# Kernel tuning notes

Measured on AMD Instinct MI355X. Metric: run time of the kernel, lower is better.

The kernel has to match this reference:

```python
import jax, jax.numpy as jnp
import numpy as np

B, V, E, H, L = 1024, 50257, 512, 512, 2


def setup_inputs() -> dict:
    key = jax.random.key(0)
    ks = jax.random.split(key, 12)
    s = 1.0 / np.sqrt(H)
    inp = {
        "x": jax.random.randint(ks[0], (B,), 0, V),
        "hidden": jnp.zeros((2 * L, B, H), jnp.float32),
        "embed": jax.random.normal(ks[1], (V, E), jnp.float32) * 0.02,
        # layer 0: input size E; layer 1: input size 2H (bidirectional concat)
        "Wih0": jax.random.uniform(ks[2], (2, 3 * H, E), jnp.float32, -s, s),
        "Whh0": jax.random.uniform(ks[3], (2, 3 * H, H), jnp.float32, -s, s),
        "bih0": jax.random.uniform(ks[4], (2, 3 * H), jnp.float32, -s, s),
        "bhh0": jax.random.uniform(ks[5], (2, 3 * H), jnp.float32, -s, s),
        "Wih1": jax.random.uniform(ks[6], (2, 3 * H, 2 * H), jnp.float32, -s, s),
        "Whh1": jax.random.uniform(ks[7], (2, 3 * H, H), jnp.float32, -s, s),
        "bih1": jax.random.uniform(ks[8], (2, 3 * H), jnp.float32, -s, s),
        "bhh1": jax.random.uniform(ks[9], (2, 3 * H), jnp.float32, -s, s),
        "Wproj": jax.random.uniform(ks[10], (V, E), jnp.float32, -1.0 / np.sqrt(E), 1.0 / np.sqrt(E)),
        "bproj": jax.random.uniform(ks[11], (V,), jnp.float32, -1.0 / np.sqrt(E), 1.0 / np.sqrt(E)),
    }
    return inp


def _gru_cell(x, h, Wih, Whh, bih, bhh):
    # PyTorch GRU cell: gates ordered (r, z, n)
    gi = x @ Wih.T + bih            # [B, 3H]
    gh = h @ Whh.T + bhh            # [B, 3H]
    ir, iz, inn = jnp.split(gi, 3, axis=-1)
    hr, hz, hn = jnp.split(gh, 3, axis=-1)
    r = jax.nn.sigmoid(ir + hr)
    z = jax.nn.sigmoid(iz + hz)
    n = jnp.tanh(inn + r * hn)
    return (1.0 - z) * n + z * h


def reference(x, hidden, embed, Wih0, Whh0, bih0, bhh0, Wih1, Whh1, bih1, bhh1, Wproj, bproj):
    inp = embed[x]                  # [B, E] embedding lookup; seq_len == 1
    layer_params = [(Wih0, Whh0, bih0, bhh0), (Wih1, Whh1, bih1, bhh1)]
    new_h = []
    for l, (Wih, Whh, bih, bhh) in enumerate(layer_params):
        # single timestep: fwd and bwd directions each do one cell step on the same input
        hf = _gru_cell(inp, hidden[2 * l],     Wih[0], Whh[0], bih[0], bhh[0])
        hb = _gru_cell(inp, hidden[2 * l + 1], Wih[1], Whh[1], bih[1], bhh[1])
        new_h += [hf, hb]
        inp = jnp.concatenate([hf, hb], axis=-1)   # [B, 2H]
    # x[:, :, hidden_dim:] -> backward-direction output of top layer, then transpose(0,1)
    out = hb[:, None, :]                            # [B, 1, H]
    logits = out @ Wproj.T + bproj                  # [B, 1, V]
    probs = jax.nn.softmax(logits, axis=-1)
    return probs, jnp.stack(new_h, axis=0)          # ([B,1,V], [2L, B, H])
```

## Files before the change

### kernel.cpp

```cpp
#include <hip/hip_runtime.h>


#define Bsz 1024
#define Hs  512
#define Vv  50257
#define VP  50304
#define NG  1536
#define NPB 393

typedef __bf16 bf16x8 __attribute__((ext_vector_type(8)));
typedef float  floatx4 __attribute__((ext_vector_type(4)));

__device__ __forceinline__ unsigned short f2bf(float f) {
  unsigned int u = __builtin_bit_cast(unsigned int, f);
  u += 0x7fffu + ((u >> 16) & 1u);
  return (unsigned short)(u >> 16);
}

__device__ __forceinline__ float bf2f(unsigned short u) {
  unsigned int x = (unsigned int)u << 16;
  return __builtin_bit_cast(float, x);
}

__device__ __forceinline__ void cvt4(const float* src, unsigned short* dst) {
  float4 f = *(const float4*)src;
  unsigned int lo = (unsigned int)f2bf(f.x) | ((unsigned int)f2bf(f.y) << 16);
  unsigned int hi = (unsigned int)f2bf(f.z) | ((unsigned int)f2bf(f.w) << 16);
  *(uint2*)dst = make_uint2(lo, hi);
}

__device__ __forceinline__ void g2lds16(const void* g, void* l) {
  unsigned long long gv = (unsigned long long)g;
  unsigned int lv = (unsigned int)(unsigned long long)l;
  __builtin_amdgcn_global_load_lds(
      (const __attribute__((address_space(1))) unsigned int*)gv,
      (__attribute__((address_space(3))) unsigned int*)lv,
      16, 0, 0);
}

__device__ __forceinline__ void gemm_core8(const unsigned short* A, const unsigned short* Bw, int K,
                                           int mt, int nt,
                                           unsigned short* Alds, unsigned short* Blds,
                                           floatx4 (&acc)[4][4]) {
  const int tid = threadIdx.x;
  const int w = tid >> 6, l = tid & 63;
  const int wr = w >> 1, wc = w & 1;
  const int g = l >> 4, r16 = l & 15;
  floatx4 zero = {0.f, 0.f, 0.f, 0.f};
#pragma unroll
  for (int i = 0; i < 4; ++i)
#pragma unroll
    for (int j = 0; j < 4; ++j) acc[i][j] = zero;

  const int nsteps = K >> 6;
  for (int kt = 0; kt < nsteps; ++kt) {
    __syncthreads();
#pragma unroll
    for (int i = 0; i < 4; ++i) {
      int chunk = w * 4 + i;
      int t16 = chunk * 64 + l;
      int row = t16 >> 3, c = t16 & 7;
      int sc = c ^ (row & 7);
      g2lds16(A + (size_t)(mt * 256 + row) * K + kt * 64 + sc * 8, (char*)Alds + chunk * 1024);
    }
#pragma unroll
    for (int i = 0; i < 2; ++i) {
      int chunk = w * 2 + i;
      int t16 = chunk * 64 + l;
      int row = t16 >> 3, c = t16 & 7;
      int sc = c ^ (row & 7);
      g2lds16(Bw + (size_t)(nt * 128 + row) * K + kt * 64 + sc * 8, (char*)Blds + chunk * 1024);
    }
    __syncthreads();
#pragma unroll
    for (int ks = 0; ks < 2; ++ks) {
      bf16x8 a[4], b[4];
#pragma unroll
      for (int i = 0; i < 4; ++i) {
        int rowA = wr * 64 + i * 16 + r16;
        int ca = (ks * 4 + g) ^ (rowA & 7);
        a[i] = *(const bf16x8*)((const char*)Alds + rowA * 128 + ca * 16);
        int rowB = wc * 64 + i * 16 + r16;
        int cb = (ks * 4 + g) ^ (rowB & 7);
        b[i] = *(const bf16x8*)((const char*)Blds + rowB * 128 + cb * 16);
      }
#pragma unroll
      for (int i = 0; i < 4; ++i)
#pragma unroll
        for (int j = 0; j < 4; ++j)
          acc[i][j] = __builtin_amdgcn_mfma_f32_16x16x32_bf16(a[i], b[j], acc[i][j], 0, 0, 0);
    }
  }
}

struct GemmDesc {
  const unsigned short* A[4];
  const unsigned short* Bw[4];
  const float* bias[4];
  float* C[4];
  int K[4];
};

__global__ __launch_bounds__(512, 4) void gemm_gru_batch(GemmDesc d) {
  __shared__ alignas(16) unsigned short Alds[256 * 64];
  __shared__ alignas(16) unsigned short Blds[128 * 64];
  const int z = blockIdx.z;
  floatx4 acc[4][4];
  gemm_core8(d.A[z], d.Bw[z], d.K[z], blockIdx.y, blockIdx.x, Alds, Blds, acc);
  const float* bias = d.bias[z];
  float* C = d.C[z];
  const int tid = threadIdx.x, w = tid >> 6, l = tid & 63;
  const int wr = w >> 1, wc = w & 1, g = l >> 4, r16 = l & 15;
#pragma unroll
  for (int i = 0; i < 4; ++i)
#pragma unroll
    for (int j = 0; j < 4; ++j) {
      int col = blockIdx.x * 128 + wc * 64 + j * 16 + r16;
      float bc = bias[col];
#pragma unroll
      for (int q = 0; q < 4; ++q) {
        int row = blockIdx.y * 256 + wr * 64 + i * 16 + g * 4 + q;
        C[(size_t)row * NG + col] = acc[i][j][q] + bc;
      }
    }
}

template <int MODE>
__global__ __launch_bounds__(512, 4) void gemm_proj(const unsigned short* A, const unsigned short* Bw,
                                                    const float* biasp, unsigned short* stash,
                                                    float* probs, float* partial, const float* inv) {
  __shared__ alignas(16) unsigned short Alds[256 * 64];
  __shared__ alignas(16) unsigned short Blds[128 * 64];
  __shared__ float rowpart[256];
  const int tid = threadIdx.x;
  if (MODE != 2 && tid < 256) rowpart[tid] = 0.f;
  int orig = blockIdx.x;
  int xcd = orig & 7, slot = orig >> 3;
  int wgid = (xcd < 4 ? xcd * 197 : 788 + (xcd - 4) * 196) + slot;
  int mt = wgid & 3, nt = wgid >> 2;
  floatx4 acc[4][4];
  gemm_core8(A, Bw, 512, mt, nt, Alds, Blds, acc);
  const int w = tid >> 6, l = tid & 63;
  const int wr = w >> 1, wc = w & 1, g = l >> 4, r16 = l & 15;
  float bcol[4];
#pragma unroll
  for (int j = 0; j < 4; ++j) bcol[j] = biasp[nt * 128 + wc * 64 + j * 16 + r16];
#pragma unroll
  for (int i = 0; i < 4; ++i)
#pragma unroll
    for (int q = 0; q < 4; ++q) {
      int rowl = wr * 64 + i * 16 + g * 4 + q;
      int grow = mt * 256 + rowl;
      float rinv = (MODE == 2) ? inv[grow] : 0.f;
      float s = 0.f;
#pragma unroll
      for (int j = 0; j < 4; ++j) {
        int col = nt * 128 + wc * 64 + j * 16 + r16;
        float v = __expf(acc[i][j][q] + bcol[j]);
        if (MODE == 0) stash[(size_t)grow * VP + col] = f2bf(v);
        if (MODE == 2) { if (col < Vv) probs[(size_t)grow * Vv + col] = v * rinv; }
        s += v;
      }
      if (MODE != 2) {
        s += __shfl_xor(s, 1); s += __shfl_xor(s, 2);
        s += __shfl_xor(s, 4); s += __shfl_xor(s, 8);
        if (r16 == 0) atomicAdd(&rowpart[rowl], s);
      }
    }
  if (MODE != 2) {
    __syncthreads();
    if (tid < 256) partial[(size_t)(mt * 256 + tid) * NPB + nt] = rowpart[tid];
  }
}

__global__ __launch_bounds__(256) void gru_gates(const float* Cbuf, const float* hidden,
                                                 float* out_newh, unsigned short* bf_out, int layer) {
  int idx = blockIdx.x * 256 + threadIdx.x;
  int j = idx & 511;
  int b = (idx >> 9) & 1023;
  int d = idx >> 19;
  const float* GI = Cbuf + (size_t)d * Bsz * NG;
  const float* GH = Cbuf + (size_t)(2 + d) * Bsz * NG;
  size_t base = (size_t)b * NG + j;
  float ir = GI[base], iz = GI[base + 512], inn = GI[base + 1024];
  float hr = GH[base], hz = GH[base + 512], hn = GH[base + 1024];
  float r = 1.f / (1.f + __expf(-(ir + hr)));
  float z = 1.f / (1.f + __expf(-(iz + hz)));
  float n = tanhf(inn + r * hn);
  size_t hoff = (size_t)(2 * layer + d) * (Bsz * Hs) + (size_t)b * Hs + j;
  float hprev = hidden[hoff];
  float h = (1.f - z) * n + z * hprev;
  out_newh[hoff] = h;
  if (layer == 0) {
    bf_out[(size_t)b * 1024 + d * 512 + j] = f2bf(h);
  } else if (d == 1) {
    bf_out[(size_t)b * 512 + j] = f2bf(h);
  }
}

__global__ void convert_all(const float* Wih0, const float* Whh0, const float* Wih1, const float* Whh1,
                            const float* hidden, const float* Wproj, const float* bproj,
                            unsigned short* wih0b, unsigned short* whh0b, unsigned short* wih1b,
                            unsigned short* whh1b, unsigned short* hbf, unsigned short* wprojb,
                            float* bprojp) {
  long long idx = ((long long)blockIdx.x * 256 + threadIdx.x) * 4;
  if (idx < 1572864) { cvt4(Wih0 + idx, wih0b + idx); return; }
  idx -= 1572864;
  if (idx < 1572864) { cvt4(Whh0 + idx, whh0b + idx); return; }
  idx -= 1572864;
  if (idx < 3145728) { cvt4(Wih1 + idx, wih1b + idx); return; }
  idx -= 3145728;
  if (idx < 1572864) { cvt4(Whh1 + idx, whh1b + idx); return; }
  idx -= 1572864;
  if (idx < 2097152) { cvt4(hidden + idx, hbf + idx); return; }
  idx -= 2097152;
  if (idx < 25755648) {
    long long row = idx >> 9, col = idx & 511;
    if (row < Vv) cvt4(Wproj + row * 512 + col, wprojb + idx);
    else *(uint2*)(wprojb + idx) = make_uint2(0u, 0u);
    return;
  }
  idx -= 25755648;
  if (idx < VP) {
    float4 v;
    v.x = (idx + 0 < Vv) ? bproj[idx + 0] : -1e30f;
    v.y = (idx + 1 < Vv) ? bproj[idx + 1] : -1e30f;
    v.z = (idx + 2 < Vv) ? bproj[idx + 2] : -1e30f;
    v.w = (idx + 3 < Vv) ? bproj[idx + 3] : -1e30f;
    *(float4*)(bprojp + idx) = v;
  }
}

__global__ void gather_embed(const int* x, const float* embed, unsigned short* xe) {
  int b = blockIdx.x, t = threadIdx.x;
  int tok = x[b];
  float2 v = *(const float2*)(embed + (size_t)tok * 512 + t * 2);
  unsigned int o = ((unsigned int)f2bf(v.y) << 16) | f2bf(v.x);
  *(unsigned int*)((unsigned short*)xe + (size_t)b * 512 + t * 2) = o;
}

__global__ void rowsum_inv(const float* partial, float* inv) {
  int row = blockIdx.x, tid = threadIdx.x;
  float s = 0.f;
  for (int c = tid; c < NPB; c += 128) s += partial[(size_t)row * NPB + c];
  __shared__ float tmp[128];
  tmp[tid] = s;
  __syncthreads();
  for (int off = 64; off > 0; off >>= 1) {
    if (tid < off) tmp[tid] += tmp[tid + off];
    __syncthreads();
  }
  if (tid == 0) inv[row] = 1.0f / tmp[0];
}

__global__ __launch_bounds__(256) void scale_expand(const unsigned short* stash, const float* inv,
                                                    float* probs) {
  const unsigned int nquad = 12865792u;
  const unsigned int step = gridDim.x * 256u;
  for (unsigned int f = blockIdx.x * 256u + threadIdx.x; f < nquad; f += step) {
    unsigned int e0 = f * 4u;
    unsigned int row = e0 / (unsigned int)Vv;
    int col = (int)(e0 - row * (unsigned int)Vv);
    float4 o;
    if (col + 4 <= Vv) {
      float s = inv[row];
      const unsigned short* sp = stash + (size_t)row * VP + col;
      if ((col & 1) == 0) {
        unsigned int u0 = *(const unsigned int*)sp;
        unsigned int u1 = *(const unsigned int*)(sp + 2);
        o.x = bf2f((unsigned short)u0) * s;
        o.y = bf2f((unsigned short)(u0 >> 16)) * s;
        o.z = bf2f((unsigned short)u1) * s;
        o.w = bf2f((unsigned short)(u1 >> 16)) * s;
      } else {
        o.x = bf2f(sp[0]) * s; o.y = bf2f(sp[1]) * s;
        o.z = bf2f(sp[2]) * s; o.w = bf2f(sp[3]) * s;
      }
    } else {
      float vals[4];
#pragma unroll
      for (int k = 0; k < 4; ++k) {
        unsigned int e = e0 + k;
        unsigned int rk = e / (unsigned int)Vv;
        int ck = (int)(e - rk * (unsigned int)Vv);
        vals[k] = bf2f(stash[(size_t)rk * VP + ck]) * inv[rk];
      }
      o.x = vals[0]; o.y = vals[1]; o.z = vals[2]; o.w = vals[3];
    }
    *(float4*)(probs + e0) = o;
  }
}

extern "C" void kernel_launch(void* const* d_in, const int* in_sizes, int n_in,
                              void* d_out, int out_size, void* d_ws, size_t ws_size,
                              hipStream_t stream) {
  const int*   x      = (const int*)d_in[0];
  const float* hidden = (const float*)d_in[1];
  const float* embed  = (const float*)d_in[2];
  const float* Wih0   = (const float*)d_in[3];
  const float* Whh0   = (const float*)d_in[4];
  const float* bih0   = (const float*)d_in[5];
  const float* bhh0   = (const float*)d_in[6];
  const float* Wih1   = (const float*)d_in[7];
  const float* Whh1   = (const float*)d_in[8];
  const float* bih1   = (const float*)d_in[9];
  const float* bhh1   = (const float*)d_in[10];
  const float* Wproj  = (const float*)d_in[11];
  const float* bproj  = (const float*)d_in[12];
  float* out = (float*)d_out;

  char* ws = (char*)d_ws;
  unsigned short* wih0b  = (unsigned short*)(ws);
  unsigned short* whh0b  = (unsigned short*)(ws + 3145728);
  unsigned short* wih1b  = (unsigned short*)(ws + 6291456);
  unsigned short* whh1b  = (unsigned short*)(ws + 12582912);
  unsigned short* hbf    = (unsigned short*)(ws + 15728640);
  unsigned short* wprojb = (unsigned short*)(ws + 19922944);
  float*          bprojp = (float*)(ws + 71434240);
  unsigned short* xe     = (unsigned short*)(ws + 71635456);
  unsigned short* inp1   = (unsigned short*)(ws + 72684032);
  unsigned short* hb1    = (unsigned short*)(ws + 74781184);
  float*          Cbuf   = (float*)(ws + 75829760);
  float*          partial= (float*)(ws + 100995584);
  float*          inv    = (float*)(ws + 102605312);
  unsigned short* stash  = (unsigned short*)(ws + 102609408);
  const size_t NEED_STASH = 102609408ull + (size_t)Bsz * VP * 2ull;

  float* out_newh = out + 51463168ll;

  convert_all<<<34930, 256, 0, stream>>>(Wih0, Whh0, Wih1, Whh1, hidden, Wproj, bproj,
                                         wih0b, whh0b, wih1b, whh1b, hbf, wprojb, bprojp);
  gather_embed<<<1024, 256, 0, stream>>>(x, embed, xe);

  GemmDesc d0;
  d0.A[0] = xe;  d0.A[1] = xe;
  d0.A[2] = hbf; d0.A[3] = hbf + 524288;
  d0.Bw[0] = wih0b; d0.Bw[1] = wih0b + 786432;
  d0.Bw[2] = whh0b; d0.Bw[3] = whh0b + 786432;
  d0.bias[0] = bih0; d0.bias[1] = bih0 + 1536;
  d0.bias[2] = bhh0; d0.bias[3] = bhh0 + 1536;
  d0.C[0] = Cbuf;             d0.C[1] = Cbuf + 1572864;
  d0.C[2] = Cbuf + 2*1572864; d0.C[3] = Cbuf + 3*1572864;
  d0.K[0] = d0.K[1] = d0.K[2] = d0.K[3] = 512;
  gemm_gru_batch<<<dim3(12, 4, 4), 512, 0, stream>>>(d0);
  gru_gates<<<4096, 256, 0, stream>>>(Cbuf, hidden, out_newh, inp1, 0);

  GemmDesc d1;
  d1.A[0] = inp1; d1.A[1] = inp1;
  d1.A[2] = hbf + 2*524288; d1.A[3] = hbf + 3*524288;
  d1.Bw[0] = wih1b; d1.Bw[1] = wih1b + 1572864;
  d1.Bw[2] = whh1b; d1.Bw[3] = whh1b + 786432;
  d1.bias[0] = bih1; d1.bias[1] = bih1 + 1536;
  d1.bias[2] = bhh1; d1.bias[3] = bhh1 + 1536;
  d1.C[0] = Cbuf;             d1.C[1] = Cbuf + 1572864;
  d1.C[2] = Cbuf + 2*1572864; d1.C[3] = Cbuf + 3*1572864;
  d1.K[0] = d1.K[1] = 1024; d1.K[2] = d1.K[3] = 512;
  gemm_gru_batch<<<dim3(12, 4, 4), 512, 0, stream>>>(d1);
  gru_gates<<<4096, 256, 0, stream>>>(Cbuf, hidden, out_newh, hb1, 1);

  if (ws_size >= NEED_STASH) {
    gemm_proj<0><<<1572, 512, 0, stream>>>(hb1, wprojb, bprojp, stash, out, partial, inv);
    rowsum_inv<<<1024, 128, 0, stream>>>(partial, inv);
    scale_expand<<<8192, 256, 0, stream>>>(stash, inv, out);
  } else {
    gemm_proj<1><<<1572, 512, 0, stream>>>(hb1, wprojb, bprojp, stash, out, partial, inv);
    rowsum_inv<<<1024, 128, 0, stream>>>(partial, inv);
    gemm_proj<2><<<1572, 512, 0, stream>>>(hb1, wprojb, bprojp, stash, out, partial, inv);
  }
}
```

Before: 252.6 us.

## Convert fp32 weights to bf16 inside GEMM with double-buffered LDS pipeline

Drops the separate pass that converts every weight matrix (including the large projection matrix) to bf16 in workspace. The GEMM B tiles are now read as fp32 into registers, converted, and written to LDS inside the main loop. The loop is double-buffered so the next tile's loads overlap the current tile's MFMA work. This saves a full read and write of roughly 100MB of weights, but doubles LDS use per block (occupancy bound lowered from 4 to 2) and doubles global read bytes for B tiles in the GEMM.

Measured after the change: 285.7 us. 1.13x slower.

```diff
diff --git a/kernel.cpp b/kernel.cpp
--- a/kernel.cpp
+++ b/kernel.cpp
@@ -38,10 +38,75 @@
       16, 0, 0);
 }
 
-__device__ __forceinline__ void gemm_core8(const unsigned short* A, const unsigned short* Bw, int K,
-                                           int mt, int nt,
-                                           unsigned short* Alds, unsigned short* Blds,
-                                           floatx4 (&acc)[4][4]) {
+__device__ __forceinline__ void stage_issueA(const unsigned short* A, int K, int mt, int kt,
+                                             unsigned short* Abuf, int w, int l) {
+#pragma unroll
+  for (int i = 0; i < 4; ++i) {
+    int chunk = w * 4 + i;
+    int t16 = chunk * 64 + l;
+    int row = t16 >> 3, c = t16 & 7;
+    int sc = c ^ (row & 7);
+    g2lds16(A + (size_t)(mt * 256 + row) * K + kt * 64 + sc * 8, (char*)Abuf + chunk * 1024);
+  }
+}
+
+__device__ __forceinline__ void stage_loadB(const float* Bw, int K, int nt, int kt, int maxrow,
+                                            float4 (&regs)[2][2], int w, int l) {
+#pragma unroll
+  for (int i = 0; i < 2; ++i) {
+    int chunk = w * 2 + i;
+    int t16 = chunk * 64 + l;
+    int row = t16 >> 3, c = t16 & 7;
+    int sc = c ^ (row & 7);
+    int rg = nt * 128 + row;
+    if (rg > maxrow) rg = maxrow;
+    const float* src = Bw + (size_t)rg * K + kt * 64 + sc * 8;
+    regs[i][0] = *(const float4*)src;
+    regs[i][1] = *(const float4*)(src + 4);
+  }
+}
+
+__device__ __forceinline__ void stage_writeB(const float4 (&regs)[2][2], unsigned short* Bbuf,
+                                             int w, int l) {
+#pragma unroll
+  for (int i = 0; i < 2; ++i) {
+    int chunk = w * 2 + i;
+    uint4 p;
+    p.x = (unsigned int)f2bf(regs[i][0].x) | ((unsigned int)f2bf(regs[i][0].y) << 16);
+    p.y = (unsigned int)f2bf(regs[i][0].z) | ((unsigned int)f2bf(regs[i][0].w) << 16);
+    p.z = (unsigned int)f2bf(regs[i][1].x) | ((unsigned int)f2bf(regs[i][1].y) << 16);
+    p.w = (unsigned int)f2bf(regs[i][1].z) | ((unsigned int)f2bf(regs[i][1].w) << 16);
+    *(uint4*)((char*)Bbuf + chunk * 1024 + l * 16) = p;
+  }
+}
+
+__device__ __forceinline__ void compute_step(const unsigned short* Acur, const unsigned short* Bcur,
+                                             floatx4 (&acc)[4][4], int wr, int wc, int g, int r16) {
+#pragma unroll
+  for (int ks = 0; ks < 2; ++ks) {
+    bf16x8 a[4], b[4];
+#pragma unroll
+    for (int i = 0; i < 4; ++i) {
+      int rowA = wr * 64 + i * 16 + r16;
+      int ca = (ks * 4 + g) ^ (rowA & 7);
+      a[i] = *(const bf16x8*)((const char*)Acur + rowA * 128 + ca * 16);
+      int rowB = wc * 64 + i * 16 + r16;
+      int cb = (ks * 4 + g) ^ (rowB & 7);
+      b[i] = *(const bf16x8*)((const char*)Bcur + rowB * 128 + cb * 16);
+    }
+#pragma unroll
+    for (int i = 0; i < 4; ++i)
+#pragma unroll
+      for (int j = 0; j < 4; ++j)
+        acc[i][j] = __builtin_amdgcn_mfma_f32_16x16x32_bf16(a[i], b[j], acc[i][j], 0, 0, 0);
+  }
+}
+
+__device__ __forceinline__ void gemm_core_db(const unsigned short* A, const float* Bw, int K,
+                                             int mt, int nt, int maxrowB,
+                                             unsigned short (&Alds)[2][16384],
+                                             unsigned short (&Blds)[2][8192],
+                                             floatx4 (&acc)[4][4]) {
   const int tid = threadIdx.x;
   const int w = tid >> 6, l = tid & 63;
   const int wr = w >> 1, wc = w & 1;
@@ -53,60 +118,39 @@
     for (int j = 0; j < 4; ++j) acc[i][j] = zero;
 
   const int nsteps = K >> 6;
+  float4 regs[2][2];
+  stage_issueA(A, K, mt, 0, Alds[0], w, l);
+  stage_loadB(Bw, K, nt, 0, maxrowB, regs, w, l);
+  stage_writeB(regs, Blds[0], w, l);
+  __syncthreads();
+  int cur = 0;
   for (int kt = 0; kt < nsteps; ++kt) {
+    const bool pf = (kt + 1 < nsteps);
+    if (pf) {
+      stage_issueA(A, K, mt, kt + 1, Alds[cur ^ 1], w, l);
+      stage_loadB(Bw, K, nt, kt + 1, maxrowB, regs, w, l);
+    }
+    compute_step(Alds[cur], Blds[cur], acc, wr, wc, g, r16);
+    if (pf) stage_writeB(regs, Blds[cur ^ 1], w, l);
     __syncthreads();
-#pragma unroll
-    for (int i = 0; i < 4; ++i) {
-      int chunk = w * 4 + i;
-      int t16 = chunk * 64 + l;
-      int row = t16 >> 3, c = t16 & 7;
-      int sc = c ^ (row & 7);
-      g2lds16(A + (size_t)(mt * 256 + row) * K + kt * 64 + sc * 8, (char*)Alds + chunk * 1024);
-    }
-#pragma unroll
-    for (int i = 0; i < 2; ++i) {
-      int chunk = w * 2 + i;
-      int t16 = chunk * 64 + l;
-      int row = t16 >> 3, c = t16 & 7;
-      int sc = c ^ (row & 7);
-      g2lds16(Bw + (size_t)(nt * 128 + row) * K + kt * 64 + sc * 8, (char*)Blds + chunk * 1024);
-    }
-    __syncthreads();
-#pragma unroll
-    for (int ks = 0; ks < 2; ++ks) {
-      bf16x8 a[4], b[4];
-#pragma unroll
-      for (int i = 0; i < 4; ++i) {
-        int rowA = wr * 64 + i * 16 + r16;
-        int ca = (ks * 4 + g) ^ (rowA & 7);
-        a[i] = *(const bf16x8*)((const char*)Alds + rowA * 128 + ca * 16);
-        int rowB = wc * 64 + i * 16 + r16;
-        int cb = (ks * 4 + g) ^ (rowB & 7);
-        b[i] = *(const bf16x8*)((const char*)Blds + rowB * 128 + cb * 16);
-      }
-#pragma unroll
-      for (int i = 0; i < 4; ++i)
-#pragma unroll
-        for (int j = 0; j < 4; ++j)
-          acc[i][j] = __builtin_amdgcn_mfma_f32_16x16x32_bf16(a[i], b[j], acc[i][j], 0, 0, 0);
-    }
+    cur ^= 1;
   }
 }
 
 struct GemmDesc {
   const unsigned short* A[4];
-  const unsigned short* Bw[4];
+  const float* Bw[4];
   const float* bias[4];
   float* C[4];
   int K[4];
 };
 
-__global__ __launch_bounds__(512, 4) void gemm_gru_batch(GemmDesc d) {
-  __shared__ alignas(16) unsigned short Alds[256 * 64];
-  __shared__ alignas(16) unsigned short Blds[128 * 64];
+__global__ __launch_bounds__(512, 2) void gemm_gru_batch(GemmDesc d) {
+  __shared__ alignas(16) unsigned short Alds[2][16384];
+  __shared__ alignas(16) unsigned short Blds[2][8192];
   const int z = blockIdx.z;
   floatx4 acc[4][4];
-  gemm_core8(d.A[z], d.Bw[z], d.K[z], blockIdx.y, blockIdx.x, Alds, Blds, acc);
+  gemm_core_db(d.A[z], d.Bw[z], d.K[z], blockIdx.y, blockIdx.x, NG - 1, Alds, Blds, acc);
   const float* bias = d.bias[z];
   float* C = d.C[z];
   const int tid = threadIdx.x, w = tid >> 6, l = tid & 63;
@@ -126,11 +170,11 @@
 }
 
 template <int MODE>
-__global__ __launch_bounds__(512, 4) void gemm_proj(const unsigned short* A, const unsigned short* Bw,
+__global__ __launch_bounds__(512, 2) void gemm_proj(const unsigned short* A, const float* Bw,
                                                     const float* biasp, unsigned short* stash,
                                                     float* probs, float* partial, const float* inv) {
-  __shared__ alignas(16) unsigned short Alds[256 * 64];
-  __shared__ alignas(16) unsigned short Blds[128 * 64];
+  __shared__ alignas(16) unsigned short Alds[2][16384];
+  __shared__ alignas(16) unsigned short Blds[2][8192];
   __shared__ float rowpart[256];
   const int tid = threadIdx.x;
   if (MODE != 2 && tid < 256) rowpart[tid] = 0.f;
@@ -139,7 +183,7 @@
   int wgid = (xcd < 4 ? xcd * 197 : 788 + (xcd - 4) * 196) + slot;
   int mt = wgid & 3, nt = wgid >> 2;
   floatx4 acc[4][4];
-  gemm_core8(A, Bw, 512, mt, nt, Alds, Blds, acc);
+  gemm_core_db(A, Bw, 512, mt, nt, Vv - 1, Alds, Blds, acc);
   const int w = tid >> 6, l = tid & 63;
   const int wr = w >> 1, wc = w & 1, g = l >> 4, r16 = l & 15;
   float bcol[4];
@@ -198,29 +242,11 @@
   }
 }
 
-__global__ void convert_all(const float* Wih0, const float* Whh0, const float* Wih1, const float* Whh1,
-                            const float* hidden, const float* Wproj, const float* bproj,
-                            unsigned short* wih0b, unsigned short* whh0b, unsigned short* wih1b,
-                            unsigned short* whh1b, unsigned short* hbf, unsigned short* wprojb,
-                            float* bprojp) {
+__global__ void convert_small(const float* hidden, const float* bproj,
+                              unsigned short* hbf, float* bprojp) {
   long long idx = ((long long)blockIdx.x * 256 + threadIdx.x) * 4;
-  if (idx < 1572864) { cvt4(Wih0 + idx, wih0b + idx); return; }
-  idx -= 1572864;
-  if (idx < 1572864) { cvt4(Whh0 + idx, whh0b + idx); return; }
-  idx -= 1572864;
-  if (idx < 3145728) { cvt4(Wih1 + idx, wih1b + idx); return; }
-  idx -= 3145728;
-  if (idx < 1572864) { cvt4(Whh1 + idx, whh1b + idx); return; }
-  idx -= 1572864;
   if (idx < 2097152) { cvt4(hidden + idx, hbf + idx); return; }
   idx -= 2097152;
-  if (idx < 25755648) {
-    long long row = idx >> 9, col = idx & 511;
-    if (row < Vv) cvt4(Wproj + row * 512 + col, wprojb + idx);
-    else *(uint2*)(wprojb + idx) = make_uint2(0u, 0u);
-    return;
-  }
-  idx -= 25755648;
   if (idx < VP) {
     float4 v;
     v.x = (idx + 0 < Vv) ? bproj[idx + 0] : -1e30f;
@@ -310,33 +336,27 @@
   float* out = (float*)d_out;
 
   char* ws = (char*)d_ws;
-  unsigned short* wih0b  = (unsigned short*)(ws);
-  unsigned short* whh0b  = (unsigned short*)(ws + 3145728);
-  unsigned short* wih1b  = (unsigned short*)(ws + 6291456);
-  unsigned short* whh1b  = (unsigned short*)(ws + 12582912);
-  unsigned short* hbf    = (unsigned short*)(ws + 15728640);
-  unsigned short* wprojb = (unsigned short*)(ws + 19922944);
-  float*          bprojp = (float*)(ws + 71434240);
-  unsigned short* xe     = (unsigned short*)(ws + 71635456);
-  unsigned short* inp1   = (unsigned short*)(ws + 72684032);
-  unsigned short* hb1    = (unsigned short*)(ws + 74781184);
-  float*          Cbuf   = (float*)(ws + 75829760);
-  float*          partial= (float*)(ws + 100995584);
-  float*          inv    = (float*)(ws + 102605312);
-  unsigned short* stash  = (unsigned short*)(ws + 102609408);
-  const size_t NEED_STASH = 102609408ull + (size_t)Bsz * VP * 2ull;
+  unsigned short* hbf    = (unsigned short*)(ws);
+  float*          bprojp = (float*)(ws + 4194304);
+  unsigned short* xe     = (unsigned short*)(ws + 4395520);
+  unsigned short* inp1   = (unsigned short*)(ws + 5444096);
+  unsigned short* hb1    = (unsigned short*)(ws + 7541248);
+  float*          Cbuf   = (float*)(ws + 8589824);
+  float*          partial= (float*)(ws + 33755648);
+  float*          inv    = (float*)(ws + 35365376);
+  unsigned short* stash  = (unsigned short*)(ws + 35369472);
+  const size_t NEED_STASH = 35369472ull + (size_t)Bsz * VP * 2ull;
 
   float* out_newh = out + 51463168ll;
 
-  convert_all<<<34930, 256, 0, stream>>>(Wih0, Whh0, Wih1, Whh1, hidden, Wproj, bproj,
-                                         wih0b, whh0b, wih1b, whh1b, hbf, wprojb, bprojp);
+  convert_small<<<2098, 256, 0, stream>>>(hidden, bproj, hbf, bprojp);
   gather_embed<<<1024, 256, 0, stream>>>(x, embed, xe);
 
   GemmDesc d0;
   d0.A[0] = xe;  d0.A[1] = xe;
   d0.A[2] = hbf; d0.A[3] = hbf + 524288;
-  d0.Bw[0] = wih0b; d0.Bw[1] = wih0b + 786432;
-  d0.Bw[2] = whh0b; d0.Bw[3] = whh0b + 786432;
+  d0.Bw[0] = Wih0; d0.Bw[1] = Wih0 + 786432;
+  d0.Bw[2] = Whh0; d0.Bw[3] = Whh0 + 786432;
   d0.bias[0] = bih0; d0.bias[1] = bih0 + 1536;
   d0.bias[2] = bhh0; d0.bias[3] = bhh0 + 1536;
   d0.C[0] = Cbuf;             d0.C[1] = Cbuf + 1572864;
@@ -348,8 +368,8 @@
   GemmDesc d1;
   d1.A[0] = inp1; d1.A[1] = inp1;
   d1.A[2] = hbf + 2*524288; d1.A[3] = hbf + 3*524288;
-  d1.Bw[0] = wih1b; d1.Bw[1] = wih1b + 1572864;
-  d1.Bw[2] = whh1b; d1.Bw[3] = whh1b + 786432;
+  d1.Bw[0] = Wih1; d1.Bw[1] = Wih1 + 1572864;
+  d1.Bw[2] = Whh1; d1.Bw[3] = Whh1 + 786432;
   d1.bias[0] = bih1; d1.bias[1] = bih1 + 1536;
   d1.bias[2] = bhh1; d1.bias[3] = bhh1 + 1536;
   d1.C[0] = Cbuf;             d1.C[1] = Cbuf + 1572864;
@@ -359,12 +379,12 @@
   gru_gates<<<4096, 256, 0, stream>>>(Cbuf, hidden, out_newh, hb1, 1);
 
   if (ws_size >= NEED_STASH) {
-    gemm_proj<0><<<1572, 512, 0, stream>>>(hb1, wprojb, bprojp, stash, out, partial, inv);
+    gemm_proj<0><<<1572, 512, 0, stream>>>(hb1, Wproj, bprojp, stash, out, partial, inv);
     rowsum_inv<<<1024, 128, 0, stream>>>(partial, inv);
     scale_expand<<<8192, 256, 0, stream>>>(stash, inv, out);
   } else {
-    gemm_proj<1><<<1572, 512, 0, stream>>>(hb1, wprojb, bprojp, stash, out, partial, inv);
+    gemm_proj<1><<<1572, 512, 0, stream>>>(hb1, Wproj, bprojp, stash, out, partial, inv);
     rowsum_inv<<<1024, 128, 0, stream>>>(partial, inv);
-    gemm_proj<2><<<1572, 512, 0, stream>>>(hb1, wprojb, bprojp, stash, out, partial, inv);
-  }
-}
+    gemm_proj<2><<<1572, 512, 0, stream>>>(hb1, Wproj, bprojp, stash, out, partial, inv);
+  }
+}
```
